# Kernel optimization log

Measured on AMD Instinct MI355X. Metric: run time of the kernel, lower is better.

The kernel has to match this reference:

```python
import jax, jax.numpy as jnp
import numpy as np

B, N, D_IN, D_OUT, E = 2, 50000, 64, 64, 800000
EPS = 0.0


def setup_inputs() -> dict:
    key = jax.random.key(0)
    ks = jax.random.split(key, 6)
    x = jax.random.normal(ks[0], (B, N, D_IN), dtype=jnp.float32)
    edge_index = jax.random.randint(ks[1], (2, E), 0, N, dtype=jnp.int64)
    # Linear params stored as [in, out] so y = h @ W + b (same math as torch Linear)
    W1 = jax.random.normal(ks[2], (D_IN, D_OUT), dtype=jnp.float32) * (1.0 / np.sqrt(D_IN))
    b1 = jax.random.normal(ks[3], (D_OUT,), dtype=jnp.float32) * 0.01
    W2 = jax.random.normal(ks[4], (D_OUT, D_OUT), dtype=jnp.float32) * (1.0 / np.sqrt(D_OUT))
    b2 = jax.random.normal(ks[5], (D_OUT,), dtype=jnp.float32) * 0.01
    return {"x": x, "edge_index": edge_index, "W1": W1, "b1": b1, "W2": W2, "b2": b2}


def reference(x, edge_index, W1, b1, W2, b2):
    src, dst = edge_index[0], edge_index[1]
    # GIN aggregation: agg[b, d] += x[b, s] for every edge (s, d), vectorized
    # gather messages [B, E, D] then scatter-add into [B, N, D]
    agg = jnp.zeros_like(x).at[:, dst].add(x[:, src])
    h = (1.0 + EPS) * x + agg
    h = jax.nn.relu(h @ W1 + b1)
    out = h @ W2 + b2
    return out
```

## Files before the change

kernel.cpp:

```cpp
#include <hip/hip_runtime.h>


#define N_NODES 50000
#define N_EDGES 800000
#define DIM 64
#define NROWS (2 * N_NODES)
#define CAP 64

#define WS_BF16_NEEDED 19400704u
#define WS_CAP_NEEDED  13000704u

typedef __attribute__((ext_vector_type(8))) short bf16x8;
typedef __attribute__((ext_vector_type(4))) float f32x4;

__device__ __forceinline__ float rlanef(float v, int l) {
    return __int_as_float(__builtin_amdgcn_readlane(__float_as_int(v), l));
}
__device__ __forceinline__ short f2bf(float f) {
    unsigned u = __float_as_uint(f);
    return (short)((u + 0x7FFFu + ((u >> 16) & 1u)) >> 16);
}
__device__ __forceinline__ unsigned pack2bf(float lo, float hi) {
    return (unsigned)(unsigned short)f2bf(lo) | ((unsigned)(unsigned short)f2bf(hi) << 16);
}

__global__ __launch_bounds__(256)
void k_fill_cap_cvt(const int* __restrict__ ei, const float* __restrict__ x,
                    unsigned* __restrict__ counts,
                    unsigned short* __restrict__ adj,
                    unsigned* __restrict__ xbp) {
    const int tid = blockIdx.x * 256 + threadIdx.x;

    const float4 f0 = reinterpret_cast<const float4*>(x)[tid * 2];
    const float4 f1 = reinterpret_cast<const float4*>(x)[tid * 2 + 1];
    uint4 p;
    p.x = pack2bf(f0.x, f0.y);
    p.y = pack2bf(f0.z, f0.w);
    p.z = pack2bf(f1.x, f1.y);
    p.w = pack2bf(f1.z, f1.w);
    reinterpret_cast<uint4*>(xbp)[tid] = p;

    if (tid < N_EDGES) {
        int s = ei[tid];
        int d = ei[N_EDGES + tid];
        unsigned pos = atomicAdd(&counts[d], 1u);
        if (pos < CAP) adj[(size_t)d * CAP + pos] = (unsigned short)s;
    }
}

__global__ __launch_bounds__(256, 8)
void k_gather_cap_bf16(const float* __restrict__ x,
                       const unsigned* __restrict__ xbp,
                       const unsigned* __restrict__ counts,
                       const unsigned short* __restrict__ adj,
                       float* __restrict__ out) {
    const int t = threadIdx.x;
    const int lane = t & 63;
    const int wave = t >> 6;
    const int node0 = (blockIdx.x * 4 + wave) * 4;

    const int half = lane >> 5;
    const int dpq  = lane & 31;
    const size_t bro = (size_t)half * N_NODES;

#define ULO(u) __uint_as_float((u) << 16)
#define UHI(u) __uint_as_float((u) & 0xFFFF0000u)

    #pragma unroll
    for (int j = 0; j < 4; ++j) {
        const int d = node0 + j;
        unsigned c = counts[d];
        if (c > (unsigned)CAP) c = CAP;
        unsigned iv = 0u;
        if ((unsigned)lane < c)
            iv = (unsigned)adj[(size_t)d * CAP + lane];

        const float2 sv = *reinterpret_cast<const float2*>(
            x + (bro + (size_t)d) * DIM + dpq * 2);
        float ax = sv.x, ay = sv.y;

        for (unsigned k = 0; k < c; k += 8u) {
            const unsigned i0 = (unsigned)__builtin_amdgcn_readlane((int)iv, k);
            const unsigned i1 = (unsigned)__builtin_amdgcn_readlane((int)iv, k + 1);
            const unsigned i2 = (unsigned)__builtin_amdgcn_readlane((int)iv, k + 2);
            const unsigned i3 = (unsigned)__builtin_amdgcn_readlane((int)iv, k + 3);
            const unsigned i4 = (unsigned)__builtin_amdgcn_readlane((int)iv, k + 4);
            const unsigned i5 = (unsigned)__builtin_amdgcn_readlane((int)iv, k + 5);
            const unsigned i6 = (unsigned)__builtin_amdgcn_readlane((int)iv, k + 6);
            const unsigned i7 = (unsigned)__builtin_amdgcn_readlane((int)iv, k + 7);
            unsigned u0 = xbp[(bro + (size_t)i0) * 32 + dpq];
            unsigned u1 = xbp[(bro + (size_t)i1) * 32 + dpq];
            unsigned u2 = xbp[(bro + (size_t)i2) * 32 + dpq];
            unsigned u3 = xbp[(bro + (size_t)i3) * 32 + dpq];
            unsigned u4 = xbp[(bro + (size_t)i4) * 32 + dpq];
            unsigned u5 = xbp[(bro + (size_t)i5) * 32 + dpq];
            unsigned u6 = xbp[(bro + (size_t)i6) * 32 + dpq];
            unsigned u7 = xbp[(bro + (size_t)i7) * 32 + dpq];
            if (k + 1u >= c) u1 = 0u;
            if (k + 2u >= c) u2 = 0u;
            if (k + 3u >= c) u3 = 0u;
            if (k + 4u >= c) u4 = 0u;
            if (k + 5u >= c) u5 = 0u;
            if (k + 6u >= c) u6 = 0u;
            if (k + 7u >= c) u7 = 0u;
            ax += ((ULO(u0) + ULO(u1)) + (ULO(u2) + ULO(u3)))
                + ((ULO(u4) + ULO(u5)) + (ULO(u6) + ULO(u7)));
            ay += ((UHI(u0) + UHI(u1)) + (UHI(u2) + UHI(u3)))
                + ((UHI(u4) + UHI(u5)) + (UHI(u6) + UHI(u7)));
        }

        float2 r; r.x = ax; r.y = ay;
        *reinterpret_cast<float2*>(out + (bro + (size_t)d) * DIM + dpq * 2) = r;
    }
#undef ULO
#undef UHI
}

#define LPAD 72

__global__ __launch_bounds__(512)
void k_mlp_mfma(float* __restrict__ buf,
                const float* __restrict__ W1, const float* __restrict__ b1,
                const float* __restrict__ W2, const float* __restrict__ b2) {
    __shared__ short w1T[DIM * LPAD];
    __shared__ short w2T[DIM * LPAD];
    __shared__ float b1s[DIM], b2s[DIM];
    __shared__ short hT[8 * 16 * LPAD];

    const int t = threadIdx.x;
    for (int i = t; i < DIM * DIM; i += 512) {
        const int k = i >> 6, n = i & 63;
        w1T[n * LPAD + k] = f2bf(W1[i]);
        w2T[n * LPAD + k] = f2bf(W2[i]);
    }
    if (t < DIM) { b1s[t] = b1[t]; b2s[t] = b2[t]; }
    __syncthreads();

    const int lane = t & 63;
    const int wave = t >> 6;
    const int base = (blockIdx.x * 8 + wave) * 16;
    if (base >= NROWS) return;

    short* __restrict__ hw = hT + wave * 16 * LPAD;
    const int arow = lane & 15;
    const int kb   = (lane >> 4) * 8;
    const int crow = (lane >> 4) * 4;

    const float* hp = buf + (size_t)(base + arow) * DIM + kb;
    float4 u0 = *(const float4*)(hp);
    float4 u1 = *(const float4*)(hp + 4);
    float4 u2 = *(const float4*)(hp + 32);
    float4 u3 = *(const float4*)(hp + 36);
    bf16x8 a0, a1;
    a0[0] = f2bf(u0.x); a0[1] = f2bf(u0.y); a0[2] = f2bf(u0.z); a0[3] = f2bf(u0.w);
    a0[4] = f2bf(u1.x); a0[5] = f2bf(u1.y); a0[6] = f2bf(u1.z); a0[7] = f2bf(u1.w);
    a1[0] = f2bf(u2.x); a1[1] = f2bf(u2.y); a1[2] = f2bf(u2.z); a1[3] = f2bf(u2.w);
    a1[4] = f2bf(u3.x); a1[5] = f2bf(u3.y); a1[6] = f2bf(u3.z); a1[7] = f2bf(u3.w);

    #pragma unroll
    for (int nt = 0; nt < 4; ++nt) {
        const int col = nt * 16 + arow;
        const bf16x8 b0 = *(const bf16x8*)(w1T + col * LPAD + kb);
        const bf16x8 b1f = *(const bf16x8*)(w1T + col * LPAD + kb + 32);
        f32x4 acc = {0.f, 0.f, 0.f, 0.f};
        acc = __builtin_amdgcn_mfma_f32_16x16x32_bf16(a0, b0, acc, 0, 0, 0);
        acc = __builtin_amdgcn_mfma_f32_16x16x32_bf16(a1, b1f, acc, 0, 0, 0);
        const float bv = b1s[col];
        #pragma unroll
        for (int r = 0; r < 4; ++r) {
            float hv = fmaxf(acc[r] + bv, 0.0f);
            hw[(crow + r) * LPAD + col] = f2bf(hv);
        }
    }

    asm volatile("s_waitcnt lgkmcnt(0)" ::: "memory");
    __builtin_amdgcn_sched_barrier(0);

    const bf16x8 c0 = *(const bf16x8*)(hw + arow * LPAD + kb);
    const bf16x8 c1 = *(const bf16x8*)(hw + arow * LPAD + kb + 32);
    #pragma unroll
    for (int nt = 0; nt < 4; ++nt) {
        const int col = nt * 16 + arow;
        const bf16x8 b0 = *(const bf16x8*)(w2T + col * LPAD + kb);
        const bf16x8 b1f = *(const bf16x8*)(w2T + col * LPAD + kb + 32);
        f32x4 acc = {0.f, 0.f, 0.f, 0.f};
        acc = __builtin_amdgcn_mfma_f32_16x16x32_bf16(c0, b0, acc, 0, 0, 0);
        acc = __builtin_amdgcn_mfma_f32_16x16x32_bf16(c1, b1f, acc, 0, 0, 0);
        const float bv = b2s[col];
        #pragma unroll
        for (int r = 0; r < 4; ++r)
            buf[(size_t)(base + crow + r) * DIM + col] = acc[r] + bv;
    }
}

__global__ __launch_bounds__(256)
void k_fill_cap(const int* __restrict__ ei, unsigned* __restrict__ counts,
                unsigned* __restrict__ adj) {
    int e = blockIdx.x * 256 + threadIdx.x;
    if (e >= N_EDGES) return;
    int s = ei[e];
    int d = ei[N_EDGES + e];
    unsigned pos = atomicAdd(&counts[d], 1u);
    if (pos < CAP) adj[(size_t)d * CAP + pos] = (unsigned)s;
}

__global__ __launch_bounds__(256, 8)
void k_gather_cap(const float* __restrict__ x,
                  const unsigned* __restrict__ counts,
                  const unsigned* __restrict__ adj,
                  float* __restrict__ out) {
    const int t = threadIdx.x;
    const int lane = t & 63;
    const int wave = t >> 6;
    const int node0 = (blockIdx.x * 4 + wave) * 4;
    const float* __restrict__ xb1 = x + (size_t)N_NODES * DIM;

    #pragma unroll
    for (int j = 0; j < 4; ++j) {
        const int d = node0 + j;
        unsigned c = counts[d];
        if (c > (unsigned)CAP) c = CAP;
        unsigned iv = adj[(size_t)d * CAP + lane];
        if ((unsigned)lane >= c) iv = 0u;

        float a0 = x[(size_t)d * DIM + lane];
        float a1 = xb1[(size_t)d * DIM + lane];

        for (unsigned k = 0; k < c; k += 8u) {
            const unsigned i0 = (unsigned)__builtin_amdgcn_readlane((int)iv, k);
            const unsigned i1 = (unsigned)__builtin_amdgcn_readlane((int)iv, k + 1);
            const unsigned i2 = (unsigned)__builtin_amdgcn_readlane((int)iv, k + 2);
            const unsigned i3 = (unsigned)__builtin_amdgcn_readlane((int)iv, k + 3);
            const unsigned i4 = (unsigned)__builtin_amdgcn_readlane((int)iv, k + 4);
            const unsigned i5 = (unsigned)__builtin_amdgcn_readlane((int)iv, k + 5);
            const unsigned i6 = (unsigned)__builtin_amdgcn_readlane((int)iv, k + 6);
            const unsigned i7 = (unsigned)__builtin_amdgcn_readlane((int)iv, k + 7);
            float v00 = x[(size_t)i0 * DIM + lane];
            float v01 = x[(size_t)i1 * DIM + lane];
            float v02 = x[(size_t)i2 * DIM + lane];
            float v03 = x[(size_t)i3 * DIM + lane];
            float v04 = x[(size_t)i4 * DIM + lane];
            float v05 = x[(size_t)i5 * DIM + lane];
            float v06 = x[(size_t)i6 * DIM + lane];
            float v07 = x[(size_t)i7 * DIM + lane];
            float v10 = xb1[(size_t)i0 * DIM + lane];
            float v11 = xb1[(size_t)i1 * DIM + lane];
            float v12 = xb1[(size_t)i2 * DIM + lane];
            float v13 = xb1[(size_t)i3 * DIM + lane];
            float v14 = xb1[(size_t)i4 * DIM + lane];
            float v15 = xb1[(size_t)i5 * DIM + lane];
            float v16 = xb1[(size_t)i6 * DIM + lane];
            float v17 = xb1[(size_t)i7 * DIM + lane];
            if (k + 1u >= c) { v01 = 0.f; v11 = 0.f; }
            if (k + 2u >= c) { v02 = 0.f; v12 = 0.f; }
            if (k + 3u >= c) { v03 = 0.f; v13 = 0.f; }
            if (k + 4u >= c) { v04 = 0.f; v14 = 0.f; }
            if (k + 5u >= c) { v05 = 0.f; v15 = 0.f; }
            if (k + 6u >= c) { v06 = 0.f; v16 = 0.f; }
            if (k + 7u >= c) { v07 = 0.f; v17 = 0.f; }
            a0 += ((v00 + v01) + (v02 + v03)) + ((v04 + v05) + (v06 + v07));
            a1 += ((v10 + v11) + (v12 + v13)) + ((v14 + v15) + (v16 + v17));
        }
        out[(size_t)d * DIM + lane] = a0;
        out[(size_t)(N_NODES + d) * DIM + lane] = a1;
    }
}

__global__ __launch_bounds__(256)
void gin_scatter(const float* __restrict__ x, const int* __restrict__ ei,
                 float* __restrict__ agg) {
    unsigned tid = blockIdx.x * 256u + threadIdx.x;
    unsigned e = tid >> 5;
    if (e >= N_EDGES) return;
    unsigned d = (tid & 31u) * 2u;
    int s = ei[e];
    int dst = ei[N_EDGES + e];
    const float2 v0 = *reinterpret_cast<const float2*>(x + (size_t)s * DIM + d);
    float* a0 = agg + (size_t)dst * DIM + d;
    unsafeAtomicAdd(a0, v0.x);
    unsafeAtomicAdd(a0 + 1, v0.y);
    const float2 v1 = *reinterpret_cast<const float2*>(x + (size_t)(N_NODES + s) * DIM + d);
    float* a1 = agg + (size_t)(N_NODES + dst) * DIM + d;
    unsafeAtomicAdd(a1, v1.x);
    unsafeAtomicAdd(a1 + 1, v1.y);
}

__global__ __launch_bounds__(256)
void gin_mlp(float* __restrict__ buf,
             const float* __restrict__ W1, const float* __restrict__ b1,
             const float* __restrict__ W2, const float* __restrict__ b2) {
    __shared__ float w1s[DIM * DIM];
    __shared__ float w2s[DIM * DIM];
    __shared__ float b1sF[DIM], b2sF[DIM];
    const int t = threadIdx.x;
    for (int i = t; i < 1024; i += 256) {
        reinterpret_cast<float4*>(w1s)[i] = reinterpret_cast<const float4*>(W1)[i];
        reinterpret_cast<float4*>(w2s)[i] = reinterpret_cast<const float4*>(W2)[i];
    }
    if (t < DIM) { b1sF[t] = b1[t]; b2sF[t] = b2[t]; }
    __syncthreads();
    const int lane = t & 63;
    const int wave = t >> 6;
    const size_t row0 = ((size_t)blockIdx.x * 4 + wave) * 8;
    float xr[8], h[8], o[8];
    #pragma unroll
    for (int j = 0; j < 8; ++j) xr[j] = buf[(row0 + j) * DIM + lane];
    #pragma unroll
    for (int j = 0; j < 8; ++j) h[j] = b1sF[lane];
    #pragma unroll
    for (int k = 0; k < DIM; ++k) {
        float w = w1s[k * DIM + lane];
        #pragma unroll
        for (int j = 0; j < 8; ++j) h[j] = fmaf(rlanef(xr[j], k), w, h[j]);
    }
    #pragma unroll
    for (int j = 0; j < 8; ++j) h[j] = fmaxf(h[j], 0.0f);
    #pragma unroll
    for (int j = 0; j < 8; ++j) o[j] = b2sF[lane];
    #pragma unroll
    for (int k = 0; k < DIM; ++k) {
        float w = w2s[k * DIM + lane];
        #pragma unroll
        for (int j = 0; j < 8; ++j) o[j] = fmaf(rlanef(h[j], k), w, o[j]);
    }
    #pragma unroll
    for (int j = 0; j < 8; ++j) buf[(row0 + j) * DIM + lane] = o[j];
}

extern "C" void kernel_launch(void* const* d_in, const int* in_sizes, int n_in,
                              void* d_out, int out_size, void* d_ws, size_t ws_size,
                              hipStream_t stream) {
    const float* x  = (const float*)d_in[0];
    const int*   ei = (const int*)d_in[1];
    const float* W1 = (const float*)d_in[2];
    const float* b1 = (const float*)d_in[3];
    const float* W2 = (const float*)d_in[4];
    const float* b2 = (const float*)d_in[5];
    float* out = (float*)d_out;

    if (ws_size >= WS_BF16_NEEDED) {
        unsigned*       counts = (unsigned*)d_ws;
        unsigned short* adj16  = (unsigned short*)((char*)d_ws + 200704);
        unsigned*       xbp    = (unsigned*)((char*)d_ws + 6600704);
        hipMemsetAsync(counts, 0, N_NODES * sizeof(unsigned), stream);
        k_fill_cap_cvt<<<3125, 256, 0, stream>>>(ei, x, counts, adj16, xbp);
        k_gather_cap_bf16<<<N_NODES / 16, 256, 0, stream>>>(x, xbp, counts, adj16, out);
        k_mlp_mfma<<<(NROWS + 127) / 128, 512, 0, stream>>>(out, W1, b1, W2, b2);
    } else if (ws_size >= WS_CAP_NEEDED) {
        unsigned* counts = (unsigned*)d_ws;
        unsigned* adj    = (unsigned*)((char*)d_ws + 200704);
        hipMemsetAsync(counts, 0, N_NODES * sizeof(unsigned), stream);
        k_fill_cap<<<(N_EDGES + 255) / 256, 256, 0, stream>>>(ei, counts, adj);
        k_gather_cap<<<N_NODES / 16, 256, 0, stream>>>(x, counts, adj, out);
        k_mlp_mfma<<<(NROWS + 127) / 128, 512, 0, stream>>>(out, W1, b1, W2, b2);
    } else {
        hipMemcpyAsync(out, x, sizeof(float) * (size_t)NROWS * DIM,
                       hipMemcpyDeviceToDevice, stream);
        gin_scatter<<<(N_EDGES * 32 + 255) / 256, 256, 0, stream>>>(x, ei, out);
        gin_mlp<<<NROWS / 32, 256, 0, stream>>>(out, W1, b1, W2, b2);
    }
}
```

Measured before the change: 107.3 us.

## Split adjacency build into 8 partitions to cut atomic contention, add overflow list

The CSR-like fill now keeps 8 separate count and adjacency arrays, chosen by block index, each capped at 16 slots, so atomics on per-node counters are spread across 8 copies. Edges that overflow a partition slot go to a small global overflow list, which a single-block fixup kernel applies with atomics after the gather. The gather walks all 8 partitions for 4 nodes per wave, reading bf16 neighbor rows. In exchange it adds a larger memset, more count and adjacency reads, an extra kernel launch, and an overflow list capped at 511 entries, beyond which edges would be dropped silently.

```diff
diff --git a/kernel.cpp b/kernel.cpp
--- a/kernel.cpp
+++ b/kernel.cpp
@@ -5,17 +5,14 @@
 #define N_EDGES 800000
 #define DIM 64
 #define NROWS (2 * N_NODES)
-#define CAP 64
-
+#define CAP8 16
+
+#define WS_X8_NEEDED   27202560u
 #define WS_BF16_NEEDED 19400704u
-#define WS_CAP_NEEDED  13000704u
 
 typedef __attribute__((ext_vector_type(8))) short bf16x8;
 typedef __attribute__((ext_vector_type(4))) float f32x4;
 
-__device__ __forceinline__ float rlanef(float v, int l) {
-    return __int_as_float(__builtin_amdgcn_readlane(__float_as_int(v), l));
-}
 __device__ __forceinline__ short f2bf(float f) {
     unsigned u = __float_as_uint(f);
     return (short)((u + 0x7FFFu + ((u >> 16) & 1u)) >> 16);
@@ -25,10 +22,11 @@
 }
 
 __global__ __launch_bounds__(256)
-void k_fill_cap_cvt(const int* __restrict__ ei, const float* __restrict__ x,
-                    unsigned* __restrict__ counts,
-                    unsigned short* __restrict__ adj,
-                    unsigned* __restrict__ xbp) {
+void k_fill_cap_cvt8(const int* __restrict__ ei, const float* __restrict__ x,
+                     unsigned* __restrict__ counts8,
+                     unsigned short* __restrict__ adj,
+                     unsigned* __restrict__ ovf,
+                     unsigned* __restrict__ xbp) {
     const int tid = blockIdx.x * 256 + threadIdx.x;
 
     const float4 f0 = reinterpret_cast<const float4*>(x)[tid * 2];
@@ -41,10 +39,242 @@
     reinterpret_cast<uint4*>(xbp)[tid] = p;
 
     if (tid < N_EDGES) {
+        const int s = ei[tid];
+        const int d = ei[N_EDGES + tid];
+        const unsigned px = (unsigned)blockIdx.x & 7u;
+        const unsigned pos = atomicAdd(&counts8[px * N_NODES + d], 1u);
+        if (pos < CAP8) {
+            adj[((size_t)px * N_NODES + d) * CAP8 + pos] = (unsigned short)s;
+        } else {
+            const unsigned o = atomicAdd(&ovf[0], 1u);
+            if (o < 511u) ovf[1 + o] = ((unsigned)d << 16) | (unsigned)s;
+        }
+    }
+}
+
+__global__ __launch_bounds__(256, 8)
+void k_gather_x8(const float* __restrict__ x,
+                 const unsigned* __restrict__ xbp,
+                 const unsigned* __restrict__ counts8,
+                 const unsigned short* __restrict__ adj,
+                 float* __restrict__ out) {
+    const int t = threadIdx.x;
+    const int lane = t & 63;
+    const int wave = t >> 6;
+    const int node0 = (blockIdx.x * 4 + wave) * 4;
+
+    const int half = lane >> 5;
+    const int dpq  = lane & 31;
+    const size_t bro = (size_t)half * N_NODES;
+
+    const int d0 = node0, d1 = node0 + 1, d2 = node0 + 2, d3 = node0 + 3;
+
+#define ULO(u) __uint_as_float((u) << 16)
+#define UHI(u) __uint_as_float((u) & 0xFFFF0000u)
+#define RL(v, l) ((unsigned)__builtin_amdgcn_readlane((int)(v), (int)(l)))
+
+    const float2 s0 = *reinterpret_cast<const float2*>(x + (bro + (size_t)d0) * DIM + dpq * 2);
+    const float2 s1 = *reinterpret_cast<const float2*>(x + (bro + (size_t)d1) * DIM + dpq * 2);
+    const float2 s2 = *reinterpret_cast<const float2*>(x + (bro + (size_t)d2) * DIM + dpq * 2);
+    const float2 s3 = *reinterpret_cast<const float2*>(x + (bro + (size_t)d3) * DIM + dpq * 2);
+    float ax0 = s0.x, ay0 = s0.y, ax1 = s1.x, ay1 = s1.y;
+    float ax2 = s2.x, ay2 = s2.y, ax3 = s3.x, ay3 = s3.y;
+
+    #pragma unroll 1
+    for (int px = 0; px < 8; ++px) {
+        const size_t sb = (size_t)px * N_NODES;
+        unsigned c0 = counts8[sb + d0]; if (c0 > CAP8) c0 = CAP8;
+        unsigned c1 = counts8[sb + d1]; if (c1 > CAP8) c1 = CAP8;
+        unsigned c2 = counts8[sb + d2]; if (c2 > CAP8) c2 = CAP8;
+        unsigned c3 = counts8[sb + d3]; if (c3 > CAP8) c3 = CAP8;
+
+        unsigned iv0 = 0, iv1 = 0, iv2 = 0, iv3 = 0;
+        if ((unsigned)lane < c0) iv0 = (unsigned)adj[(sb + (size_t)d0) * CAP8 + lane];
+        if ((unsigned)lane < c1) iv1 = (unsigned)adj[(sb + (size_t)d1) * CAP8 + lane];
+        if ((unsigned)lane < c2) iv2 = (unsigned)adj[(sb + (size_t)d2) * CAP8 + lane];
+        if ((unsigned)lane < c3) iv3 = (unsigned)adj[(sb + (size_t)d3) * CAP8 + lane];
+
+        for (unsigned k = 0; k < c0; k += 4u) {
+            const unsigned i0 = RL(iv0, k), i1 = RL(iv0, k + 1),
+                           i2 = RL(iv0, k + 2), i3 = RL(iv0, k + 3);
+            unsigned u0 = xbp[(bro + (size_t)i0) * 32 + dpq];
+            unsigned u1 = xbp[(bro + (size_t)i1) * 32 + dpq];
+            unsigned u2 = xbp[(bro + (size_t)i2) * 32 + dpq];
+            unsigned u3 = xbp[(bro + (size_t)i3) * 32 + dpq];
+            if (k + 1u >= c0) u1 = 0u;
+            if (k + 2u >= c0) u2 = 0u;
+            if (k + 3u >= c0) u3 = 0u;
+            ax0 += (ULO(u0) + ULO(u1)) + (ULO(u2) + ULO(u3));
+            ay0 += (UHI(u0) + UHI(u1)) + (UHI(u2) + UHI(u3));
+        }
+        for (unsigned k = 0; k < c1; k += 4u) {
+            const unsigned i0 = RL(iv1, k), i1 = RL(iv1, k + 1),
+                           i2 = RL(iv1, k + 2), i3 = RL(iv1, k + 3);
+            unsigned u0 = xbp[(bro + (size_t)i0) * 32 + dpq];
+            unsigned u1 = xbp[(bro + (size_t)i1) * 32 + dpq];
+            unsigned u2 = xbp[(bro + (size_t)i2) * 32 + dpq];
+            unsigned u3 = xbp[(bro + (size_t)i3) * 32 + dpq];
+            if (k + 1u >= c1) u1 = 0u;
+            if (k + 2u >= c1) u2 = 0u;
+            if (k + 3u >= c1) u3 = 0u;
+            ax1 += (ULO(u0) + ULO(u1)) + (ULO(u2) + ULO(u3));
+            ay1 += (UHI(u0) + UHI(u1)) + (UHI(u2) + UHI(u3));
+        }
+        for (unsigned k = 0; k < c2; k += 4u) {
+            const unsigned i0 = RL(iv2, k), i1 = RL(iv2, k + 1),
+                           i2 = RL(iv2, k + 2), i3 = RL(iv2, k + 3);
+            unsigned u0 = xbp[(bro + (size_t)i0) * 32 + dpq];
+            unsigned u1 = xbp[(bro + (size_t)i1) * 32 + dpq];
+            unsigned u2 = xbp[(bro + (size_t)i2) * 32 + dpq];
+            unsigned u3 = xbp[(bro + (size_t)i3) * 32 + dpq];
+            if (k + 1u >= c2) u1 = 0u;
+            if (k + 2u >= c2) u2 = 0u;
+            if (k + 3u >= c2) u3 = 0u;
+            ax2 += (ULO(u0) + ULO(u1)) + (ULO(u2) + ULO(u3));
+            ay2 += (UHI(u0) + UHI(u1)) + (UHI(u2) + UHI(u3));
+        }
+        for (unsigned k = 0; k < c3; k += 4u) {
+            const unsigned i0 = RL(iv3, k), i1 = RL(iv3, k + 1),
+                           i2 = RL(iv3, k + 2), i3 = RL(iv3, k + 3);
+            unsigned u0 = xbp[(bro + (size_t)i0) * 32 + dpq];
+            unsigned u1 = xbp[(bro + (size_t)i1) * 32 + dpq];
+            unsigned u2 = xbp[(bro + (size_t)i2) * 32 + dpq];
+            unsigned u3 = xbp[(bro + (size_t)i3) * 32 + dpq];
+            if (k + 1u >= c3) u1 = 0u;
+            if (k + 2u >= c3) u2 = 0u;
+            if (k + 3u >= c3) u3 = 0u;
+            ax3 += (ULO(u0) + ULO(u1)) + (ULO(u2) + ULO(u3));
+            ay3 += (UHI(u0) + UHI(u1)) + (UHI(u2) + UHI(u3));
+        }
+    }
+
+    float2 r;
+    r.x = ax0; r.y = ay0;
+    *reinterpret_cast<float2*>(out + (bro + (size_t)d0) * DIM + dpq * 2) = r;
+    r.x = ax1; r.y = ay1;
+    *reinterpret_cast<float2*>(out + (bro + (size_t)d1) * DIM + dpq * 2) = r;
+    r.x = ax2; r.y = ay2;
+    *reinterpret_cast<float2*>(out + (bro + (size_t)d2) * DIM + dpq * 2) = r;
+    r.x = ax3; r.y = ay3;
+    *reinterpret_cast<float2*>(out + (bro + (size_t)d3) * DIM + dpq * 2) = r;
+#undef ULO
+#undef UHI
+#undef RL
+}
+
+__global__ __launch_bounds__(256)
+void k_ovf_fix(const float* __restrict__ x, const unsigned* __restrict__ ovf,
+               float* __restrict__ out) {
+    const int lane = threadIdx.x & 63;
+    const int wave = threadIdx.x >> 6;
+    unsigned cnt = ovf[0];
+    if (cnt > 511u) cnt = 511u;
+    for (unsigned i = wave; i < cnt; i += 4u) {
+        const unsigned u = ovf[1 + i];
+        const unsigned d = u >> 16, s = u & 0xFFFFu;
+        unsafeAtomicAdd(&out[(size_t)d * DIM + lane],
+                        x[(size_t)s * DIM + lane]);
+        unsafeAtomicAdd(&out[(size_t)(N_NODES + d) * DIM + lane],
+                        x[(size_t)(N_NODES + s) * DIM + lane]);
+    }
+}
+
+#define LPAD 72
+
+__global__ __launch_bounds__(512)
+void k_mlp_mfma(float* __restrict__ buf,
+                const float* __restrict__ W1, const float* __restrict__ b1,
+                const float* __restrict__ W2, const float* __restrict__ b2) {
+    __shared__ short w1T[DIM * LPAD];
+    __shared__ short w2T[DIM * LPAD];
+    __shared__ float b1s[DIM], b2s[DIM];
+    __shared__ short hT[8 * 16 * LPAD];
+
+    const int t = threadIdx.x;
+    for (int i = t; i < DIM * DIM; i += 512) {
+        const int k = i >> 6, n = i & 63;
+        w1T[n * LPAD + k] = f2bf(W1[i]);
+        w2T[n * LPAD + k] = f2bf(W2[i]);
+    }
+    if (t < DIM) { b1s[t] = b1[t]; b2s[t] = b2[t]; }
+    __syncthreads();
+
+    const int lane = t & 63;
+    const int wave = t >> 6;
+    const int base = (blockIdx.x * 8 + wave) * 16;
+    if (base >= NROWS) return;
+
+    short* __restrict__ hw = hT + wave * 16 * LPAD;
+    const int arow = lane & 15;
+    const int kb   = (lane >> 4) * 8;
+    const int crow = (lane >> 4) * 4;
+
+    const float* hp = buf + (size_t)(base + arow) * DIM + kb;
+    float4 u0 = *(const float4*)(hp);
+    float4 u1 = *(const float4*)(hp + 4);
+    float4 u2 = *(const float4*)(hp + 32);
+    float4 u3 = *(const float4*)(hp + 36);
+    bf16x8 a0, a1;
+    a0[0] = f2bf(u0.x); a0[1] = f2bf(u0.y); a0[2] = f2bf(u0.z); a0[3] = f2bf(u0.w);
+    a0[4] = f2bf(u1.x); a0[5] = f2bf(u1.y); a0[6] = f2bf(u1.z); a0[7] = f2bf(u1.w);
+    a1[0] = f2bf(u2.x); a1[1] = f2bf(u2.y); a1[2] = f2bf(u2.z); a1[3] = f2bf(u2.w);
+    a1[4] = f2bf(u3.x); a1[5] = f2bf(u3.y); a1[6] = f2bf(u3.z); a1[7] = f2bf(u3.w);
+
+    #pragma unroll
+    for (int nt = 0; nt < 4; ++nt) {
+        const int col = nt * 16 + arow;
+        const bf16x8 b0 = *(const bf16x8*)(w1T + col * LPAD + kb);
+        const bf16x8 b1f = *(const bf16x8*)(w1T + col * LPAD + kb + 32);
+        f32x4 acc = {0.f, 0.f, 0.f, 0.f};
+        acc = __builtin_amdgcn_mfma_f32_16x16x32_bf16(a0, b0, acc, 0, 0, 0);
+        acc = __builtin_amdgcn_mfma_f32_16x16x32_bf16(a1, b1f, acc, 0, 0, 0);
+        const float bv = b1s[col];
+        #pragma unroll
+        for (int r = 0; r < 4; ++r) {
+            float hv = fmaxf(acc[r] + bv, 0.0f);
+            hw[(crow + r) * LPAD + col] = f2bf(hv);
+        }
+    }
+
+    asm volatile("s_waitcnt lgkmcnt(0)" ::: "memory");
+    __builtin_amdgcn_sched_barrier(0);
+
+    const bf16x8 c0 = *(const bf16x8*)(hw + arow * LPAD + kb);
+    const bf16x8 c1 = *(const bf16x8*)(hw + arow * LPAD + kb + 32);
+    #pragma unroll
+    for (int nt = 0; nt < 4; ++nt) {
+        const int col = nt * 16 + arow;
+        const bf16x8 b0 = *(const bf16x8*)(w2T + col * LPAD + kb);
+        const bf16x8 b1f = *(const bf16x8*)(w2T + col * LPAD + kb + 32);
+        f32x4 acc = {0.f, 0.f, 0.f, 0.f};
+        acc = __builtin_amdgcn_mfma_f32_16x16x32_bf16(c0, b0, acc, 0, 0, 0);
+        acc = __builtin_amdgcn_mfma_f32_16x16x32_bf16(c1, b1f, acc, 0, 0, 0);
+        const float bv = b2s[col];
+        #pragma unroll
+        for (int r = 0; r < 4; ++r)
+            buf[(size_t)(base + crow + r) * DIM + col] = acc[r] + bv;
+    }
+}
+
+__global__ __launch_bounds__(256)
+void k_fill_cap_cvt(const int* __restrict__ ei, const float* __restrict__ x,
+                    unsigned* __restrict__ counts,
+                    unsigned short* __restrict__ adj,
+                    unsigned* __restrict__ xbp) {
+    const int tid = blockIdx.x * 256 + threadIdx.x;
+    const float4 f0 = reinterpret_cast<const float4*>(x)[tid * 2];
+    const float4 f1 = reinterpret_cast<const float4*>(x)[tid * 2 + 1];
+    uint4 p;
+    p.x = pack2bf(f0.x, f0.y);
+    p.y = pack2bf(f0.z, f0.w);
+    p.z = pack2bf(f1.x, f1.y);
+    p.w = pack2bf(f1.z, f1.w);
+    reinterpret_cast<uint4*>(xbp)[tid] = p;
+    if (tid < N_EDGES) {
         int s = ei[tid];
         int d = ei[N_EDGES + tid];
         unsigned pos = atomicAdd(&counts[d], 1u);
-        if (pos < CAP) adj[(size_t)d * CAP + pos] = (unsigned short)s;
+        if (pos < 64u) adj[(size_t)d * 64 + pos] = (unsigned short)s;
     }
 }
 
@@ -58,27 +288,21 @@
     const int lane = t & 63;
     const int wave = t >> 6;
     const int node0 = (blockIdx.x * 4 + wave) * 4;
-
     const int half = lane >> 5;
     const int dpq  = lane & 31;
     const size_t bro = (size_t)half * N_NODES;
-
 #define ULO(u) __uint_as_float((u) << 16)
 #define UHI(u) __uint_as_float((u) & 0xFFFF0000u)
-
     #pragma unroll
     for (int j = 0; j < 4; ++j) {
         const int d = node0 + j;
         unsigned c = counts[d];
-        if (c > (unsigned)CAP) c = CAP;
+        if (c > 64u) c = 64u;
         unsigned iv = 0u;
-        if ((unsigned)lane < c)
-            iv = (unsigned)adj[(size_t)d * CAP + lane];
-
+        if ((unsigned)lane < c) iv = (unsigned)adj[(size_t)d * 64 + lane];
         const float2 sv = *reinterpret_cast<const float2*>(
             x + (bro + (size_t)d) * DIM + dpq * 2);
         float ax = sv.x, ay = sv.y;
-
         for (unsigned k = 0; k < c; k += 8u) {
             const unsigned i0 = (unsigned)__builtin_amdgcn_readlane((int)iv, k);
             const unsigned i1 = (unsigned)__builtin_amdgcn_readlane((int)iv, k + 1);
@@ -108,7 +332,6 @@
             ay += ((UHI(u0) + UHI(u1)) + (UHI(u2) + UHI(u3)))
                 + ((UHI(u4) + UHI(u5)) + (UHI(u6) + UHI(u7)));
         }
-
         float2 r; r.x = ax; r.y = ay;
         *reinterpret_cast<float2*>(out + (bro + (size_t)d) * DIM + dpq * 2) = r;
     }
@@ -116,154 +339,8 @@
 #undef UHI
 }
 
-#define LPAD 72
-
-__global__ __launch_bounds__(512)
-void k_mlp_mfma(float* __restrict__ buf,
-                const float* __restrict__ W1, const float* __restrict__ b1,
-                const float* __restrict__ W2, const float* __restrict__ b2) {
-    __shared__ short w1T[DIM * LPAD];
-    __shared__ short w2T[DIM * LPAD];
-    __shared__ float b1s[DIM], b2s[DIM];
-    __shared__ short hT[8 * 16 * LPAD];
-
-    const int t = threadIdx.x;
-    for (int i = t; i < DIM * DIM; i += 512) {
-        const int k = i >> 6, n = i & 63;
-        w1T[n * LPAD + k] = f2bf(W1[i]);
-        w2T[n * LPAD + k] = f2bf(W2[i]);
-    }
-    if (t < DIM) { b1s[t] = b1[t]; b2s[t] = b2[t]; }
-    __syncthreads();
-
-    const int lane = t & 63;
-    const int wave = t >> 6;
-    const int base = (blockIdx.x * 8 + wave) * 16;
-    if (base >= NROWS) return;
-
-    short* __restrict__ hw = hT + wave * 16 * LPAD;
-    const int arow = lane & 15;
-    const int kb   = (lane >> 4) * 8;
-    const int crow = (lane >> 4) * 4;
-
-    const float* hp = buf + (size_t)(base + arow) * DIM + kb;
-    float4 u0 = *(const float4*)(hp);
-    float4 u1 = *(const float4*)(hp + 4);
-    float4 u2 = *(const float4*)(hp + 32);
-    float4 u3 = *(const float4*)(hp + 36);
-    bf16x8 a0, a1;
-    a0[0] = f2bf(u0.x); a0[1] = f2bf(u0.y); a0[2] = f2bf(u0.z); a0[3] = f2bf(u0.w);
-    a0[4] = f2bf(u1.x); a0[5] = f2bf(u1.y); a0[6] = f2bf(u1.z); a0[7] = f2bf(u1.w);
-    a1[0] = f2bf(u2.x); a1[1] = f2bf(u2.y); a1[2] = f2bf(u2.z); a1[3] = f2bf(u2.w);
-    a1[4] = f2bf(u3.x); a1[5] = f2bf(u3.y); a1[6] = f2bf(u3.z); a1[7] = f2bf(u3.w);
-
-    #pragma unroll
-    for (int nt = 0; nt < 4; ++nt) {
-        const int col = nt * 16 + arow;
-        const bf16x8 b0 = *(const bf16x8*)(w1T + col * LPAD + kb);
-        const bf16x8 b1f = *(const bf16x8*)(w1T + col * LPAD + kb + 32);
-        f32x4 acc = {0.f, 0.f, 0.f, 0.f};
-        acc = __builtin_amdgcn_mfma_f32_16x16x32_bf16(a0, b0, acc, 0, 0, 0);
-        acc = __builtin_amdgcn_mfma_f32_16x16x32_bf16(a1, b1f, acc, 0, 0, 0);
-        const float bv = b1s[col];
-        #pragma unroll
-        for (int r = 0; r < 4; ++r) {
-            float hv = fmaxf(acc[r] + bv, 0.0f);
-            hw[(crow + r) * LPAD + col] = f2bf(hv);
-        }
-    }
-
-    asm volatile("s_waitcnt lgkmcnt(0)" ::: "memory");
-    __builtin_amdgcn_sched_barrier(0);
-
-    const bf16x8 c0 = *(const bf16x8*)(hw + arow * LPAD + kb);
-    const bf16x8 c1 = *(const bf16x8*)(hw + arow * LPAD + kb + 32);
-    #pragma unroll
-    for (int nt = 0; nt < 4; ++nt) {
-        const int col = nt * 16 + arow;
-        const bf16x8 b0 = *(const bf16x8*)(w2T + col * LPAD + kb);
-        const bf16x8 b1f = *(const bf16x8*)(w2T + col * LPAD + kb + 32);
-        f32x4 acc = {0.f, 0.f, 0.f, 0.f};
-        acc = __builtin_amdgcn_mfma_f32_16x16x32_bf16(c0, b0, acc, 0, 0, 0);
-        acc = __builtin_amdgcn_mfma_f32_16x16x32_bf16(c1, b1f, acc, 0, 0, 0);
-        const float bv = b2s[col];
-        #pragma unroll
-        for (int r = 0; r < 4; ++r)
-            buf[(size_t)(base + crow + r) * DIM + col] = acc[r] + bv;
-    }
-}
-
-__global__ __launch_bounds__(256)
-void k_fill_cap(const int* __restrict__ ei, unsigned* __restrict__ counts,
-                unsigned* __restrict__ adj) {
-    int e = blockIdx.x * 256 + threadIdx.x;
-    if (e >= N_EDGES) return;
-    int s = ei[e];
-    int d = ei[N_EDGES + e];
-    unsigned pos = atomicAdd(&counts[d], 1u);
-    if (pos < CAP) adj[(size_t)d * CAP + pos] = (unsigned)s;
-}
-
-__global__ __launch_bounds__(256, 8)
-void k_gather_cap(const float* __restrict__ x,
-                  const unsigned* __restrict__ counts,
-                  const unsigned* __restrict__ adj,
-                  float* __restrict__ out) {
-    const int t = threadIdx.x;
-    const int lane = t & 63;
-    const int wave = t >> 6;
-    const int node0 = (blockIdx.x * 4 + wave) * 4;
-    const float* __restrict__ xb1 = x + (size_t)N_NODES * DIM;
-
-    #pragma unroll
-    for (int j = 0; j < 4; ++j) {
-        const int d = node0 + j;
-        unsigned c = counts[d];
-        if (c > (unsigned)CAP) c = CAP;
-        unsigned iv = adj[(size_t)d * CAP + lane];
-        if ((unsigned)lane >= c) iv = 0u;
-
-        float a0 = x[(size_t)d * DIM + lane];
-        float a1 = xb1[(size_t)d * DIM + lane];
-
-        for (unsigned k = 0; k < c; k += 8u) {
-            const unsigned i0 = (unsigned)__builtin_amdgcn_readlane((int)iv, k);
-            const unsigned i1 = (unsigned)__builtin_amdgcn_readlane((int)iv, k + 1);
-            const unsigned i2 = (unsigned)__builtin_amdgcn_readlane((int)iv, k + 2);
-            const unsigned i3 = (unsigned)__builtin_amdgcn_readlane((int)iv, k + 3);
-            const unsigned i4 = (unsigned)__builtin_amdgcn_readlane((int)iv, k + 4);
-            const unsigned i5 = (unsigned)__builtin_amdgcn_readlane((int)iv, k + 5);
-            const unsigned i6 = (unsigned)__builtin_amdgcn_readlane((int)iv, k + 6);
-            const unsigned i7 = (unsigned)__builtin_amdgcn_readlane((int)iv, k + 7);
-            float v00 = x[(size_t)i0 * DIM + lane];
-            float v01 = x[(size_t)i1 * DIM + lane];
-            float v02 = x[(size_t)i2 * DIM + lane];
-            float v03 = x[(size_t)i3 * DIM + lane];
-            float v04 = x[(size_t)i4 * DIM + lane];
-            float v05 = x[(size_t)i5 * DIM + lane];
-            float v06 = x[(size_t)i6 * DIM + lane];
-            float v07 = x[(size_t)i7 * DIM + lane];
-            float v10 = xb1[(size_t)i0 * DIM + lane];
-            float v11 = xb1[(size_t)i1 * DIM + lane];
-            float v12 = xb1[(size_t)i2 * DIM + lane];
-            float v13 = xb1[(size_t)i3 * DIM + lane];
-            float v14 = xb1[(size_t)i4 * DIM + lane];
-            float v15 = xb1[(size_t)i5 * DIM + lane];
-            float v16 = xb1[(size_t)i6 * DIM + lane];
-            float v17 = xb1[(size_t)i7 * DIM + lane];
-            if (k + 1u >= c) { v01 = 0.f; v11 = 0.f; }
-            if (k + 2u >= c) { v02 = 0.f; v12 = 0.f; }
-            if (k + 3u >= c) { v03 = 0.f; v13 = 0.f; }
-            if (k + 4u >= c) { v04 = 0.f; v14 = 0.f; }
-            if (k + 5u >= c) { v05 = 0.f; v15 = 0.f; }
-            if (k + 6u >= c) { v06 = 0.f; v16 = 0.f; }
-            if (k + 7u >= c) { v07 = 0.f; v17 = 0.f; }
-            a0 += ((v00 + v01) + (v02 + v03)) + ((v04 + v05) + (v06 + v07));
-            a1 += ((v10 + v11) + (v12 + v13)) + ((v14 + v15) + (v16 + v17));
-        }
-        out[(size_t)d * DIM + lane] = a0;
-        out[(size_t)(N_NODES + d) * DIM + lane] = a1;
-    }
+__device__ __forceinline__ float rlanef(float v, int l) {
+    return __int_as_float(__builtin_amdgcn_readlane(__float_as_int(v), l));
 }
 
 __global__ __launch_bounds__(256)
@@ -338,7 +415,17 @@
     const float* b2 = (const float*)d_in[5];
     float* out = (float*)d_out;
 
-    if (ws_size >= WS_BF16_NEEDED) {
+    if (ws_size >= WS_X8_NEEDED) {
+        unsigned*       counts8 = (unsigned*)d_ws;
+        unsigned*       ovf     = (unsigned*)((char*)d_ws + 1600000);
+        unsigned short* adj16   = (unsigned short*)((char*)d_ws + 1602560);
+        unsigned*       xbp     = (unsigned*)((char*)d_ws + 14402560);
+        hipMemsetAsync(counts8, 0, 1602048, stream);
+        k_fill_cap_cvt8<<<3125, 256, 0, stream>>>(ei, x, counts8, adj16, ovf, xbp);
+        k_gather_x8<<<N_NODES / 16, 256, 0, stream>>>(x, xbp, counts8, adj16, out);
+        k_ovf_fix<<<1, 256, 0, stream>>>(x, ovf, out);
+        k_mlp_mfma<<<(NROWS + 127) / 128, 512, 0, stream>>>(out, W1, b1, W2, b2);
+    } else if (ws_size >= WS_BF16_NEEDED) {
         unsigned*       counts = (unsigned*)d_ws;
         unsigned short* adj16  = (unsigned short*)((char*)d_ws + 200704);
         unsigned*       xbp    = (unsigned*)((char*)d_ws + 6600704);
@@ -346,13 +433,6 @@
         k_fill_cap_cvt<<<3125, 256, 0, stream>>>(ei, x, counts, adj16, xbp);
         k_gather_cap_bf16<<<N_NODES / 16, 256, 0, stream>>>(x, xbp, counts, adj16, out);
         k_mlp_mfma<<<(NROWS + 127) / 128, 512, 0, stream>>>(out, W1, b1, W2, b2);
-    } else if (ws_size >= WS_CAP_NEEDED) {
-        unsigned* counts = (unsigned*)d_ws;
-        unsigned* adj    = (unsigned*)((char*)d_ws + 200704);
-        hipMemsetAsync(counts, 0, N_NODES * sizeof(unsigned), stream);
-        k_fill_cap<<<(N_EDGES + 255) / 256, 256, 0, stream>>>(ei, counts, adj);
-        k_gather_cap<<<N_NODES / 16, 256, 0, stream>>>(x, counts, adj, out);
-        k_mlp_mfma<<<(NROWS + 127) / 128, 512, 0, stream>>>(out, W1, b1, W2, b2);
     } else {
         hipMemcpyAsync(out, x, sizeof(float) * (size_t)NROWS * DIM,
                        hipMemcpyDeviceToDevice, stream);
```

Measured after the change: 115.3 us. 7.5% more time.
